# Performance work log

Hardware: AMD Instinct MI355X
Metric: run time of the kernel (lower is better)

The kernel has to match this reference:

```python
import jax, jax.numpy as jnp
import numpy as np

EPS = 1e-5
V = 65536      # number of surface vertices
E = 1048576    # number of neighbor points (~16 per vertex)
H = 128        # h_dim
CHEM_IN = 34   # 2 + num_gdf*2
GEOM_IN = 48   # num_gdf*2 + num_signatures


def _bn(x, p):
    # p: [4, dim] = (gamma, beta, running_mean, running_var); eval-mode BatchNorm1d
    g, b, m, v = p[0], p[1], p[2], p[3]
    return (x - m) * jax.lax.rsqrt(v + EPS) * g + b


def _mk_bn(key, dim):
    km, kv = jax.random.split(key)
    gamma = jnp.ones((dim,), jnp.float32)
    beta = jnp.zeros((dim,), jnp.float32)
    mean = 0.1 * jax.random.normal(km, (dim,), jnp.float32)
    var = 0.5 + jax.random.uniform(kv, (dim,), jnp.float32)  # strictly positive
    return jnp.stack([gamma, beta, mean, var])


def _mk_lin(key, din, dout):
    kw, kb = jax.random.split(key)
    s = 1.0 / np.sqrt(din)
    w = jax.random.uniform(kw, (din, dout), jnp.float32, -s, s)
    b = jax.random.uniform(kb, (dout,), jnp.float32, -s, s)
    return w, b


def setup_inputs() -> dict:
    key = jax.random.key(0)
    ks = jax.random.split(key, 16)
    chem_feats = jax.random.normal(ks[0], (E, CHEM_IN), jnp.float32)
    geom_feats = jax.random.normal(ks[1], (V, GEOM_IN), jnp.float32)
    nbr_vids = jax.random.randint(ks[2], (E,), 0, V, jnp.int64 if jax.config.jax_enable_x64 else jnp.int32)
    w1, b1 = _mk_lin(ks[3], CHEM_IN, H)
    w2, b2 = _mk_lin(ks[4], H, 2 * H)
    wg1, bg1 = _mk_lin(ks[5], GEOM_IN, H // 2)
    wg2, bg2 = _mk_lin(ks[6], H // 2, H // 2)
    wf1, bf1 = _mk_lin(ks[7], H + H // 2, H)
    wf2, bf2 = _mk_lin(ks[8], H, H)
    return {
        "chem_feats": chem_feats, "geom_feats": geom_feats, "nbr_vids": nbr_vids,
        "w1": w1, "b1": b1, "bn1": _mk_bn(ks[9], H),
        "w2": w2, "b2": b2, "bn2": _mk_bn(ks[10], 2 * H),
        "wg1": wg1, "bg1": bg1, "bng1": _mk_bn(ks[11], H // 2),
        "wg2": wg2, "bg2": bg2, "bng2": _mk_bn(ks[12], H // 2),
        "wf1": wf1, "bf1": bf1, "bnf1": _mk_bn(ks[13], H),
        "wf2": wf2, "bf2": bf2, "bnf2": _mk_bn(ks[14], H),
    }


def reference(chem_feats, geom_feats, nbr_vids,
              w1, b1, bn1, w2, b2, bn2,
              wg1, bg1, bng1, wg2, bg2, bng2,
              wf1, bf1, bnf1, wf2, bf2, bnf2):
    n_verts = geom_feats.shape[0]
    # chem_mlp: Linear -> (Dropout eval=id) -> BN -> SiLU -> Linear -> BN
    h = jax.nn.silu(_bn(chem_feats @ w1 + b1, bn1))
    h = _bn(h @ w2 + b2, bn2)                      # [E, 2H]
    nbr_filter, nbr_core = jnp.split(h, 2, axis=-1)
    h_chem = jax.nn.sigmoid(nbr_filter) * jax.nn.softplus(nbr_core)  # gated [E, H]
    h_chem = jax.ops.segment_sum(h_chem, nbr_vids, num_segments=n_verts)  # [V, H]
    # geom_mlp
    g = jax.nn.silu(_bn(geom_feats @ wg1 + bg1, bng1))
    h_geom = _bn(g @ wg2 + bg2, bng2)              # [V, H/2]
    # feat_mlp on concat
    x = jnp.concatenate([h_chem, h_geom], axis=-1)  # [V, 3H/2]
    x = jax.nn.silu(_bn(x @ wf1 + bf1, bnf1))
    h_out = _bn(x @ wf2 + bf2, bnf2)               # [V, H]
    return h_out
```

## Files before the change

### kernel.cpp

```cpp
#include <hip/hip_runtime.h>
#include <cstddef>

constexpr int V_CNT = 65536;
constexpr int E_CNT = 1048576;
constexpr int H_DIM = 128;
constexpr int CI = 34;
constexpr int GI = 48;
#define EPSF 1e-5f

typedef _Float16 f16;
typedef f16 f16x8 __attribute__((ext_vector_type(8)));
typedef float f32x4 __attribute__((ext_vector_type(4)));
#define MFMA16(a,b,c) __builtin_amdgcn_mfma_f32_16x16x32_f16(a,b,c,0,0,0)

__device__ __forceinline__ float sigmoidf_(float x){ return 1.0f/(1.0f+__expf(-x)); }
__device__ __forceinline__ float siluf_(float x){ return x/(1.0f+__expf(-x)); }
__device__ __forceinline__ float softplusf_(float x){
  return fmaxf(x,0.0f) + __logf(1.0f + __expf(-fabsf(x)));
}

__global__ __launch_bounds__(256) void prep_kernel(
    const float* __restrict__ w1, const float* __restrict__ b1, const float* __restrict__ bn1,
    const float* __restrict__ w2, const float* __restrict__ b2, const float* __restrict__ bn2,
    const float* __restrict__ wg1, const float* __restrict__ bg1, const float* __restrict__ bng1,
    const float* __restrict__ wg2, const float* __restrict__ bg2, const float* __restrict__ bng2,
    const float* __restrict__ wf1, const float* __restrict__ bf1, const float* __restrict__ bnf1,
    const float* __restrict__ wf2, const float* __restrict__ bf2, const float* __restrict__ bnf2,
    f16* __restrict__ w1f, float* __restrict__ shift1,
    f16* __restrict__ w2f, float* __restrict__ shift2,
    f16* __restrict__ wg1f, float* __restrict__ shiftg1,
    f16* __restrict__ wg2f, float* __restrict__ shiftg2,
    f16* __restrict__ wf1f, float* __restrict__ shiftf1,
    f16* __restrict__ wf2f, float* __restrict__ shiftf2)
{
  int t = blockIdx.x*256 + threadIdx.x;
  if (t < 128*64){
    int n = t>>6, k = t&63;
    float s = bn1[n]*rsqrtf(bn1[384+n]+EPSF);
    w1f[t] = (k<CI) ? (f16)(w1[k*128+n]*s) : (f16)0.f;
    if (k==0) shift1[n] = fmaf(s, b1[n]-bn1[256+n], bn1[128+n]);
  }
  if (t < 256*128){
    int n = t>>7, k = t&127;
    float s = bn2[n]*rsqrtf(bn2[768+n]+EPSF);
    w2f[t] = (f16)(w2[k*256+n]*s);
    if (k==0) shift2[n] = fmaf(s, b2[n]-bn2[512+n], bn2[256+n]);
  }
  if (t < 64*64){
    int n = t>>6, k = t&63;
    float s = bng1[n]*rsqrtf(bng1[192+n]+EPSF);
    wg1f[t] = (k<GI) ? (f16)(wg1[k*64+n]*s) : (f16)0.f;
    if (k==0) shiftg1[n] = fmaf(s, bg1[n]-bng1[128+n], bng1[64+n]);
  }
  if (t < 64*64){
    int n = t>>6, k = t&63;
    float s = bng2[n]*rsqrtf(bng2[192+n]+EPSF);
    wg2f[t] = (f16)(wg2[k*64+n]*s);
    if (k==0) shiftg2[n] = fmaf(s, bg2[n]-bng2[128+n], bng2[64+n]);
  }
  if (t < 128*192){
    int n = t/192, k = t - n*192;
    float s = bnf1[n]*rsqrtf(bnf1[384+n]+EPSF);
    wf1f[t] = (f16)(wf1[k*128+n]*s);
    if (k==0) shiftf1[n] = fmaf(s, bf1[n]-bnf1[256+n], bnf1[128+n]);
  }
  if (t < 128*128){
    int n = t>>7, k = t&127;
    float s = bnf2[n]*rsqrtf(bnf2[384+n]+EPSF);
    wf2f[t] = (f16)(wf2[k*128+n]*s);
    if (k==0) shiftf2[n] = fmaf(s, bf2[n]-bnf2[256+n], bnf2[128+n]);
  }
}

__global__ __launch_bounds__(256) void hist_kernel(const int* __restrict__ vids, int* __restrict__ counts){
  int i = blockIdx.x*blockDim.x + threadIdx.x;
  int stride = gridDim.x*blockDim.x;
  for(; i<E_CNT; i+=stride) atomicAdd(&counts[vids[i]], 1);
}

__global__ __launch_bounds__(1024) void scan_kernel(const int* __restrict__ counts,
                                                    int* __restrict__ offsets,
                                                    int* __restrict__ offsets_work){
  __shared__ int ps[1024];
  const int t = threadIdx.x;
  int4 c[16]; int s = 0;
  const int4* cp = (const int4*)counts + (size_t)t*16;
  #pragma unroll
  for(int i=0;i<16;i++){ c[i]=cp[i]; s += c[i].x+c[i].y+c[i].z+c[i].w; }
  ps[t]=s; __syncthreads();
  for(int d=1; d<1024; d<<=1){
    int v = (t>=d) ? ps[t-d] : 0;
    __syncthreads();
    ps[t] += v;
    __syncthreads();
  }
  int run = ps[t]-s;
  int4* o1 = (int4*)offsets + (size_t)t*16;
  int4* o2 = (int4*)offsets_work + (size_t)t*16;
  #pragma unroll
  for(int i=0;i<16;i++){
    int4 cc=c[i]; int4 o;
    o.x=run; run+=cc.x; o.y=run; run+=cc.y; o.z=run; run+=cc.z; o.w=run; run+=cc.w;
    o1[i]=o; o2[i]=o;
  }
  if(t==1023) offsets[65536] = run;
}

__global__ __launch_bounds__(256) void scatter_kernel(const int* __restrict__ vids,
                                                      int* __restrict__ offsets_work,
                                                      int* __restrict__ perm,
                                                      int* __restrict__ svid){
  int i = blockIdx.x*blockDim.x + threadIdx.x;
  int stride = gridDim.x*blockDim.x;
  for(; i<E_CNT; i+=stride){
    int v = vids[i];
    int pos = atomicAdd(&offsets_work[v], 1);
    perm[pos] = i;
    svid[pos] = v;
  }
}

__global__ __launch_bounds__(256) void geom_mfma(
    const float* __restrict__ geom,
    const f16* __restrict__ wg1f, const float* __restrict__ shg1,
    const f16* __restrict__ wg2f, const float* __restrict__ shg2,
    f16* __restrict__ dst, int stride, int colbase)
{
  __shared__ __align__(16) f16 Ag[64][72];
  const int t = threadIdx.x, w = t>>6, lane = t&63, n16 = lane&15, quad = lane>>4;
  const int v0 = blockIdx.x*64;
  const int col = w*16 + n16;

  for(int i=t;i<64*GI;i+=256){ int r=i/GI, k=i-r*GI; Ag[r][k] = (f16)geom[(size_t)v0*GI + i]; }
  { uint* Aw=(uint*)Ag; for(int i=t;i<64*8;i+=256){ int r=i>>3; Aw[r*36+24+(i&7)]=0u; } }

  f16x8 bg1[2], bg2[2];
  #pragma unroll
  for(int ks=0;ks<2;ks++){
    bg1[ks] = *(const f16x8*)(wg1f + (size_t)col*64 + ks*32 + quad*8);
    bg2[ks] = *(const f16x8*)(wg2f + (size_t)col*64 + ks*32 + quad*8);
  }
  __syncthreads();

  f32x4 c1[4];
  #pragma unroll
  for(int mt=0;mt<4;mt++) c1[mt] = (f32x4)(0.f);
  #pragma unroll
  for(int mt=0;mt<4;mt++)
    #pragma unroll
    for(int ks=0;ks<2;ks++){
      f16x8 a = *(const f16x8*)(&Ag[mt*16+n16][ks*32+quad*8]);
      c1[mt] = MFMA16(a, bg1[ks], c1[mt]);
    }
  __syncthreads();

  float s1 = shg1[col];
  #pragma unroll
  for(int mt=0;mt<4;mt++)
    #pragma unroll
    for(int r=0;r<4;r++)
      Ag[mt*16+quad*4+r][col] = (f16)siluf_(c1[mt][r] + s1);
  __syncthreads();

  f32x4 c2[4];
  #pragma unroll
  for(int mt=0;mt<4;mt++) c2[mt] = (f32x4)(0.f);
  #pragma unroll
  for(int mt=0;mt<4;mt++)
    #pragma unroll
    for(int ks=0;ks<2;ks++){
      f16x8 a = *(const f16x8*)(&Ag[mt*16+n16][ks*32+quad*8]);
      c2[mt] = MFMA16(a, bg2[ks], c2[mt]);
    }
  float s2 = shg2[col];
  #pragma unroll
  for(int mt=0;mt<4;mt++)
    #pragma unroll
    for(int r=0;r<4;r++)
      dst[(size_t)(v0 + mt*16+quad*4+r)*stride + colbase + col] = (f16)(c2[mt][r] + s2);
}

__global__ __launch_bounds__(256) void zero_f4(float4* p, int n4){
  int i = blockIdx.x*blockDim.x + threadIdx.x;
  int stride = gridDim.x*blockDim.x;
  float4 z; z.x=0.f; z.y=0.f; z.z=0.f; z.w=0.f;
  for(; i<n4; i+=stride) p[i] = z;
}

__global__ __launch_bounds__(256) void chem_fused(
    const float* __restrict__ chem,
    const int* __restrict__ perm, const int* __restrict__ svid,
    const f16* __restrict__ w1f, const float* __restrict__ shift1,
    const f16* __restrict__ w2f, const float* __restrict__ shift2,
    float* __restrict__ h_chem)
{
  __shared__ __align__(16) f16 A2[64][136];
  __shared__ __align__(16) f16 G[64][136];
  __shared__ int vid_s[64];
  const int t = threadIdx.x, w = t>>6, lane = t&63, n16 = lane&15, quad = lane>>4;
  const long p0 = (long)blockIdx.x*64;

  if(t<64) vid_s[t] = svid[p0+t];

  f16x8 b1[2][2];
  #pragma unroll
  for(int p=0;p<2;p++){
    int col = (2*w+p)*16 + n16;
    #pragma unroll
    for(int ks=0;ks<2;ks++)
      b1[p][ks] = *(const f16x8*)(w1f + (size_t)col*64 + ks*32 + quad*8);
  }
  float sh1v[2] = { shift1[(2*w+0)*16+n16], shift1[(2*w+1)*16+n16] };

  int pe[4];
  #pragma unroll
  for(int mt=0;mt<4;mt++) pe[mt] = perm[p0 + mt*16 + n16];

  f32x4 c1[4][2];
  #pragma unroll
  for(int mt=0;mt<4;mt++){ c1[mt][0]=(f32x4)(0.f); c1[mt][1]=(f32x4)(0.f); }
  #pragma unroll
  for(int mt=0;mt<4;mt++){
    const float* base = chem + (size_t)pe[mt]*CI;
    float2 u0 = *(const float2*)(base + quad*8 + 0);
    float2 u1 = *(const float2*)(base + quad*8 + 2);
    float2 u2 = *(const float2*)(base + quad*8 + 4);
    float2 u3 = *(const float2*)(base + quad*8 + 6);
    f16x8 a0;
    a0[0]=(f16)u0.x; a0[1]=(f16)u0.y; a0[2]=(f16)u1.x; a0[3]=(f16)u1.y;
    a0[4]=(f16)u2.x; a0[5]=(f16)u2.y; a0[6]=(f16)u3.x; a0[7]=(f16)u3.y;
    f16x8 a1 = (f16x8)(f16)0.f;
    if(quad==0){
      float2 uT = *(const float2*)(base + 32);
      a1[0]=(f16)uT.x; a1[1]=(f16)uT.y;
    }
    #pragma unroll
    for(int p=0;p<2;p++){
      c1[mt][p] = MFMA16(a0, b1[p][0], c1[mt][p]);
      c1[mt][p] = MFMA16(a1, b1[p][1], c1[mt][p]);
    }
  }
  #pragma unroll
  for(int mt=0;mt<4;mt++)
    #pragma unroll
    for(int p=0;p<2;p++){
      int col = (2*w+p)*16 + n16;
      #pragma unroll
      for(int r=0;r<4;r++)
        A2[mt*16+quad*4+r][col] = (f16)siluf_(c1[mt][p][r] + sh1v[p]);
    }
  __syncthreads();

  #pragma unroll 1
  for(int p=0;p<2;p++){
    const int gf = 2*w + p, gc = gf + 8;
    f16x8 b2f[4], b2c[4];
    #pragma unroll
    for(int ks=0;ks<4;ks++){
      b2f[ks] = *(const f16x8*)(w2f + (size_t)(gf*16+n16)*128 + ks*32 + quad*8);
      b2c[ks] = *(const f16x8*)(w2f + (size_t)(gc*16+n16)*128 + ks*32 + quad*8);
    }
    float shf = shift2[gf*16+n16];
    float shc = shift2[128 + gf*16+n16];
    f32x4 cf[4], cc_[4];
    #pragma unroll
    for(int mt=0;mt<4;mt++){ cf[mt]=(f32x4)(0.f); cc_[mt]=(f32x4)(0.f); }
    #pragma unroll
    for(int ks=0;ks<4;ks++){
      f16x8 a[4];
      #pragma unroll
      for(int mt=0;mt<4;mt++)
        a[mt] = *(const f16x8*)(&A2[mt*16+n16][ks*32+quad*8]);
      #pragma unroll
      for(int mt=0;mt<4;mt++){
        cf[mt]  = MFMA16(a[mt], b2f[ks], cf[mt]);
        cc_[mt] = MFMA16(a[mt], b2c[ks], cc_[mt]);
      }
    }
    #pragma unroll
    for(int mt=0;mt<4;mt++)
      #pragma unroll
      for(int r=0;r<4;r++){
        float f  = sigmoidf_(cf[mt][r]  + shf);
        float s  = softplusf_(cc_[mt][r] + shc);
        G[mt*16+quad*4+r][gf*16+n16] = (f16)(f*s);
      }
  }
  __syncthreads();

  {
    const int l = lane, g = w;
    const int e_beg = g*16, e_end = e_beg+16;
    float a0=0.f, a1=0.f;
    int cur = vid_s[e_beg];
    #pragma unroll 1
    for(int e=e_beg; e<e_end; ++e){
      int v = vid_s[e];
      if(v != cur){
        unsafeAtomicAdd(h_chem + (size_t)cur*H_DIM + 2*l,     a0);
        unsafeAtomicAdd(h_chem + (size_t)cur*H_DIM + 2*l + 1, a1);
        a0=0.f; a1=0.f; cur=v;
      }
      union{uint u; f16 h[2];} q;
      q.u = *(const uint*)&G[e][2*l];
      a0 += (float)q.h[0]; a1 += (float)q.h[1];
    }
    unsafeAtomicAdd(h_chem + (size_t)cur*H_DIM + 2*l,     a0);
    unsafeAtomicAdd(h_chem + (size_t)cur*H_DIM + 2*l + 1, a1);
  }
}

__global__ __launch_bounds__(256) void chem_atomic(
    const float* __restrict__ chem, const int* __restrict__ vids,
    const f16* __restrict__ w1f, const float* __restrict__ shift1,
    const f16* __restrict__ w2f, const float* __restrict__ shift2,
    float* __restrict__ h_chem)
{
  __shared__ __align__(16) f16 A2[64][136];
  __shared__ __align__(16) int vid_s[64];
  const int t = threadIdx.x, w = t>>6, lane = t&63, n16 = lane&15, quad = lane>>4;
  const long e0 = (long)blockIdx.x*64;

  if(t<64) vid_s[t] = vids[e0+t];

  f16x8 b1[2][2];
  #pragma unroll
  for(int p=0;p<2;p++){
    int col = (2*w+p)*16 + n16;
    #pragma unroll
    for(int ks=0;ks<2;ks++)
      b1[p][ks] = *(const f16x8*)(w1f + (size_t)col*64 + ks*32 + quad*8);
  }
  float sh1v[2] = { shift1[(2*w+0)*16+n16], shift1[(2*w+1)*16+n16] };

  f32x4 c1[4][2];
  #pragma unroll
  for(int mt=0;mt<4;mt++){ c1[mt][0]=(f32x4)(0.f); c1[mt][1]=(f32x4)(0.f); }
  #pragma unroll
  for(int mt=0;mt<4;mt++){
    const float* base = chem + (size_t)(e0 + mt*16 + n16)*CI;
    float2 u0 = *(const float2*)(base + quad*8 + 0);
    float2 u1 = *(const float2*)(base + quad*8 + 2);
    float2 u2 = *(const float2*)(base + quad*8 + 4);
    float2 u3 = *(const float2*)(base + quad*8 + 6);
    f16x8 a0;
    a0[0]=(f16)u0.x; a0[1]=(f16)u0.y; a0[2]=(f16)u1.x; a0[3]=(f16)u1.y;
    a0[4]=(f16)u2.x; a0[5]=(f16)u2.y; a0[6]=(f16)u3.x; a0[7]=(f16)u3.y;
    f16x8 a1 = (f16x8)(f16)0.f;
    if(quad==0){
      float2 uT = *(const float2*)(base + 32);
      a1[0]=(f16)uT.x; a1[1]=(f16)uT.y;
    }
    #pragma unroll
    for(int p=0;p<2;p++){
      c1[mt][p] = MFMA16(a0, b1[p][0], c1[mt][p]);
      c1[mt][p] = MFMA16(a1, b1[p][1], c1[mt][p]);
    }
  }
  #pragma unroll
  for(int mt=0;mt<4;mt++)
    #pragma unroll
    for(int p=0;p<2;p++){
      int col = (2*w+p)*16 + n16;
      #pragma unroll
      for(int r=0;r<4;r++)
        A2[mt*16+quad*4+r][col] = (f16)siluf_(c1[mt][p][r] + sh1v[p]);
    }
  const int ntab[4] = {2*w, 2*w+1, 2*w+8, 2*w+9};
  f16x8 b2[4][4];
  #pragma unroll
  for(int p=0;p<4;p++){
    int col = ntab[p]*16 + n16;
    #pragma unroll
    for(int ks=0;ks<4;ks++)
      b2[p][ks] = *(const f16x8*)(w2f + (size_t)col*128 + ks*32 + quad*8);
  }
  float shf[2] = { shift2[(2*w+0)*16+n16], shift2[(2*w+1)*16+n16] };
  float shc[2] = { shift2[128+(2*w+0)*16+n16], shift2[128+(2*w+1)*16+n16] };
  __syncthreads();

  f32x4 c2[4][4];
  #pragma unroll
  for(int mt=0;mt<4;mt++)
    #pragma unroll
    for(int p=0;p<4;p++) c2[mt][p] = (f32x4)(0.f);
  #pragma unroll
  for(int ks=0;ks<4;ks++){
    f16x8 a[4];
    #pragma unroll
    for(int mt=0;mt<4;mt++)
      a[mt] = *(const f16x8*)(&A2[mt*16+n16][ks*32+quad*8]);
    #pragma unroll
    for(int mt=0;mt<4;mt++)
      #pragma unroll
      for(int p=0;p<4;p++)
        c2[mt][p] = MFMA16(a[mt], b2[p][ks], c2[mt][p]);
  }
  #pragma unroll
  for(int mt=0;mt<4;mt++){
    int4 ev = *(const int4*)&vid_s[mt*16 + quad*4];
    int evv[4] = {ev.x, ev.y, ev.z, ev.w};
    #pragma unroll
    for(int p=0;p<2;p++){
      int colf = (2*w+p)*16 + n16;
      #pragma unroll
      for(int r=0;r<4;r++){
        float f  = sigmoidf_(c2[mt][p][r]   + shf[p]);
        float cc = softplusf_(c2[mt][p+2][r] + shc[p]);
        unsafeAtomicAdd(h_chem + (size_t)evv[r]*H_DIM + colf, f*cc);
      }
    }
  }
}

__global__ __launch_bounds__(256) void feat_split(
    const float* __restrict__ h_chem, const f16* __restrict__ h_geom,
    const f16* __restrict__ wf1f, const float* __restrict__ shf1,
    const f16* __restrict__ wf2f, const float* __restrict__ shf2,
    float* __restrict__ out)
{
  __shared__ __align__(16) f16 Af[64][200];
  const int t = threadIdx.x, w = t>>6, lane = t&63, n16 = lane&15, quad = lane>>4;
  const int v0 = blockIdx.x*64;

  for(int i=t;i<64*128;i+=256){ int r=i>>7, k=i&127; Af[r][k] = (f16)h_chem[(size_t)(v0+r)*128 + k]; }
  for(int i=t;i<64*64;i+=256){ int r=i>>6, k=i&63; Af[r][128+k] = h_geom[(size_t)(v0+r)*64 + k]; }

  f16x8 B1[2][6];
  #pragma unroll
  for(int p=0;p<2;p++){
    int col = (2*w+p)*16 + n16;
    #pragma unroll
    for(int ks=0;ks<6;ks++)
      B1[p][ks] = *(const f16x8*)(wf1f + (size_t)col*192 + ks*32 + quad*8);
  }
  __syncthreads();

  f32x4 c1[4][2];
  #pragma unroll
  for(int mt=0;mt<4;mt++){ c1[mt][0]=(f32x4)(0.f); c1[mt][1]=(f32x4)(0.f); }
  #pragma unroll
  for(int ks=0;ks<6;ks++){
    f16x8 a[4];
    #pragma unroll
    for(int mt=0;mt<4;mt++)
      a[mt] = *(const f16x8*)(&Af[mt*16+n16][ks*32+quad*8]);
    #pragma unroll
    for(int mt=0;mt<4;mt++)
      #pragma unroll
      for(int p=0;p<2;p++) c1[mt][p] = MFMA16(a[mt], B1[p][ks], c1[mt][p]);
  }
  __syncthreads();

  float s1v[2] = { shf1[(2*w+0)*16+n16], shf1[(2*w+1)*16+n16] };
  #pragma unroll
  for(int mt=0;mt<4;mt++)
    #pragma unroll
    for(int p=0;p<2;p++){
      int col = (2*w+p)*16 + n16;
      #pragma unroll
      for(int r=0;r<4;r++)
        Af[mt*16+quad*4+r][col] = (f16)siluf_(c1[mt][p][r] + s1v[p]);
    }
  __syncthreads();

  f16x8 B2[2][4];
  #pragma unroll
  for(int p=0;p<2;p++){
    int col = (2*w+p)*16 + n16;
    #pragma unroll
    for(int ks=0;ks<4;ks++)
      B2[p][ks] = *(const f16x8*)(wf2f + (size_t)col*128 + ks*32 + quad*8);
  }
  f32x4 c2[4][2];
  #pragma unroll
  for(int mt=0;mt<4;mt++){ c2[mt][0]=(f32x4)(0.f); c2[mt][1]=(f32x4)(0.f); }
  #pragma unroll
  for(int ks=0;ks<4;ks++){
    f16x8 a[4];
    #pragma unroll
    for(int mt=0;mt<4;mt++)
      a[mt] = *(const f16x8*)(&Af[mt*16+n16][ks*32+quad*8]);
    #pragma unroll
    for(int mt=0;mt<4;mt++)
      #pragma unroll
      for(int p=0;p<2;p++) c2[mt][p] = MFMA16(a[mt], B2[p][ks], c2[mt][p]);
  }
  float s2v[2] = { shf2[(2*w+0)*16+n16], shf2[(2*w+1)*16+n16] };
  #pragma unroll
  for(int mt=0;mt<4;mt++)
    #pragma unroll
    for(int p=0;p<2;p++){
      int col = (2*w+p)*16 + n16;
      #pragma unroll
      for(int r=0;r<4;r++)
        out[(size_t)(v0 + mt*16+quad*4+r)*128 + col] = c2[mt][p][r] + s2v[p];
    }
}

extern "C" void kernel_launch(void* const* d_in, const int* in_sizes, int n_in,
                              void* d_out, int out_size, void* d_ws, size_t ws_size,
                              hipStream_t stream) {
  const float* chem = (const float*)d_in[0];
  const float* geom = (const float*)d_in[1];
  const int*   vids = (const int*)d_in[2];
  const float* w1  = (const float*)d_in[3];
  const float* b1  = (const float*)d_in[4];
  const float* bn1 = (const float*)d_in[5];
  const float* w2  = (const float*)d_in[6];
  const float* b2  = (const float*)d_in[7];
  const float* bn2 = (const float*)d_in[8];
  const float* wg1 = (const float*)d_in[9];
  const float* bg1 = (const float*)d_in[10];
  const float* bng1= (const float*)d_in[11];
  const float* wg2 = (const float*)d_in[12];
  const float* bg2 = (const float*)d_in[13];
  const float* bng2= (const float*)d_in[14];
  const float* wf1 = (const float*)d_in[15];
  const float* bf1 = (const float*)d_in[16];
  const float* bnf1= (const float*)d_in[17];
  const float* wf2 = (const float*)d_in[18];
  const float* bf2 = (const float*)d_in[19];
  const float* bnf2= (const float*)d_in[20];
  float* out = (float*)d_out;
  char* ws = (char*)d_ws;

  const size_t NEED_BIG = 51301632ULL;
  const bool big = (ws_size >= NEED_BIG);

  if (big) {
    float* h_chem     = (float*)(ws + 0);
    f16*   h_geom     = (f16*)  (ws + 33554432);
    int*   perm       = (int*)  (ws + 41943040);
    int*   svid       = (int*)  (ws + 46137344);
    int*   counts     = (int*)  (ws + 50331648);
    int*   offsets    = (int*)  (ws + 50593792);
    int*   offsets_wk = (int*)  (ws + 50856192);
    char*  wb         = ws + 51118336;
    f16*   w1f  = (f16*)(wb);
    f16*   w2f  = (f16*)(wb + 16384);
    f16*   wg1f = (f16*)(wb + 81920);
    f16*   wg2f = (f16*)(wb + 90112);
    f16*   wf1f = (f16*)(wb + 98304);
    f16*   wf2f = (f16*)(wb + 147456);
    float* shift1  = (float*)(wb + 180224);
    float* shift2  = (float*)(wb + 180736);
    float* shiftg1 = (float*)(wb + 181760);
    float* shiftg2 = (float*)(wb + 182016);
    float* shiftf1 = (float*)(wb + 182272);
    float* shiftf2 = (float*)(wb + 182784);

    hipMemsetAsync(counts, 0, 65536*sizeof(int), stream);
    prep_kernel<<<dim3(128), dim3(256), 0, stream>>>(
        w1,b1,bn1, w2,b2,bn2, wg1,bg1,bng1, wg2,bg2,bng2, wf1,bf1,bnf1, wf2,bf2,bnf2,
        w1f,shift1, w2f,shift2, wg1f,shiftg1, wg2f,shiftg2, wf1f,shiftf1, wf2f,shiftf2);
    hist_kernel<<<dim3(1024), dim3(256), 0, stream>>>(vids, counts);
    scan_kernel<<<dim3(1), dim3(1024), 0, stream>>>(counts, offsets, offsets_wk);
    scatter_kernel<<<dim3(1024), dim3(256), 0, stream>>>(vids, offsets_wk, perm, svid);
    zero_f4<<<dim3(4096), dim3(256), 0, stream>>>((float4*)h_chem, V_CNT*H_DIM/4);
    geom_mfma<<<dim3(V_CNT/64), dim3(256), 0, stream>>>(geom, wg1f,shiftg1, wg2f,shiftg2, h_geom, 64, 0);
    chem_fused<<<dim3(E_CNT/64), dim3(256), 0, stream>>>(chem, perm, svid, w1f,shift1, w2f,shift2, h_chem);
    feat_split<<<dim3(V_CNT/64), dim3(256), 0, stream>>>(h_chem, h_geom, wf1f,shiftf1, wf2f,shiftf2, out);
  } else {
    float* h_chem = (float*)(ws + 0);
    f16*   h_geom = (f16*)  (ws + 33554432);
    char*  wb     = ws + 41943040;
    f16*   w1f  = (f16*)(wb);
    f16*   w2f  = (f16*)(wb + 16384);
    f16*   wg1f = (f16*)(wb + 81920);
    f16*   wg2f = (f16*)(wb + 90112);
    f16*   wf1f = (f16*)(wb + 98304);
    f16*   wf2f = (f16*)(wb + 147456);
    float* shift1  = (float*)(wb + 180224);
    float* shift2  = (float*)(wb + 180736);
    float* shiftg1 = (float*)(wb + 181760);
    float* shiftg2 = (float*)(wb + 182016);
    float* shiftf1 = (float*)(wb + 182272);
    float* shiftf2 = (float*)(wb + 182784);

    prep_kernel<<<dim3(128), dim3(256), 0, stream>>>(
        w1,b1,bn1, w2,b2,bn2, wg1,bg1,bng1, wg2,bg2,bng2, wf1,bf1,bnf1, wf2,bf2,bnf2,
        w1f,shift1, w2f,shift2, wg1f,shiftg1, wg2f,shiftg2, wf1f,shiftf1, wf2f,shiftf2);
    zero_f4<<<dim3(4096), dim3(256), 0, stream>>>((float4*)h_chem, V_CNT*H_DIM/4);
    geom_mfma<<<dim3(V_CNT/64), dim3(256), 0, stream>>>(geom, wg1f,shiftg1, wg2f,shiftg2, h_geom, 64, 0);
    chem_atomic<<<dim3(E_CNT/64), dim3(256), 0, stream>>>(chem, vids, w1f,shift1, w2f,shift2, h_chem);
    feat_split<<<dim3(V_CNT/64), dim3(256), 0, stream>>>(h_chem, h_geom, wf1f,shiftf1, wf2f,shiftf2, out);
  }
}
```

Measured before the change: 724.9 us.

## Fuse prep/hist/zero launches, merge geom into chem kernel, shrink feat tile

Folds weight prep, the histogram, and zeroing of h_chem into one front kernel selected by block range. The geom MLP is merged into the chem kernel as extra blocks, and the svid and offsets arrays are dropped in favour of vids[perm]. Gate results are kept in registers so the chem kernel reuses the A2 shared buffer, cutting LDS and raising occupancy. The feat kernel drops to 32-row tiles, loads use float4, and sigmoid/silu use a fast reciprocal. Fewer launches and less memory traffic are traded for an extra indirect load and slightly lower rcp precision.

Result: faster. 692.7 us (-4.4%).

```diff
diff --git a/kernel.cpp b/kernel.cpp
--- a/kernel.cpp
+++ b/kernel.cpp
@@ -13,13 +13,14 @@
 typedef float f32x4 __attribute__((ext_vector_type(4)));
 #define MFMA16(a,b,c) __builtin_amdgcn_mfma_f32_16x16x32_f16(a,b,c,0,0,0)
 
-__device__ __forceinline__ float sigmoidf_(float x){ return 1.0f/(1.0f+__expf(-x)); }
-__device__ __forceinline__ float siluf_(float x){ return x/(1.0f+__expf(-x)); }
+__device__ __forceinline__ float frcp_(float x){ return __builtin_amdgcn_rcpf(x); }
+__device__ __forceinline__ float sigmoidf_(float x){ return frcp_(1.0f+__expf(-x)); }
+__device__ __forceinline__ float siluf_(float x){ return x*frcp_(1.0f+__expf(-x)); }
 __device__ __forceinline__ float softplusf_(float x){
   return fmaxf(x,0.0f) + __logf(1.0f + __expf(-fabsf(x)));
 }
 
-__global__ __launch_bounds__(256) void prep_kernel(
+__global__ __launch_bounds__(256) void front_kernel(
     const float* __restrict__ w1, const float* __restrict__ b1, const float* __restrict__ bn1,
     const float* __restrict__ w2, const float* __restrict__ b2, const float* __restrict__ bn2,
     const float* __restrict__ wg1, const float* __restrict__ bg1, const float* __restrict__ bng1,
@@ -31,9 +32,24 @@
     f16* __restrict__ wg1f, float* __restrict__ shiftg1,
     f16* __restrict__ wg2f, float* __restrict__ shiftg2,
     f16* __restrict__ wf1f, float* __restrict__ shiftf1,
-    f16* __restrict__ wf2f, float* __restrict__ shiftf2)
+    f16* __restrict__ wf2f, float* __restrict__ shiftf2,
+    const int* __restrict__ vids, int* __restrict__ counts,
+    float4* __restrict__ h_chem_zero)
 {
-  int t = blockIdx.x*256 + threadIdx.x;
+  const int b = blockIdx.x;
+  if (b >= 1152) {
+    int i = (b-1152)*256 + threadIdx.x;
+    float4 z; z.x=0.f; z.y=0.f; z.z=0.f; z.w=0.f;
+    const int n4 = V_CNT*H_DIM/4;
+    for(; i<n4; i+=2048*256) h_chem_zero[i] = z;
+    return;
+  }
+  if (b >= 128) {
+    int i = (b-128)*256 + threadIdx.x;
+    for(; i<E_CNT; i+=1024*256) atomicAdd(&counts[vids[i]], 1);
+    return;
+  }
+  int t = b*256 + threadIdx.x;
   if (t < 128*64){
     int n = t>>6, k = t&63;
     float s = bn1[n]*rsqrtf(bn1[384+n]+EPSF);
@@ -72,14 +88,7 @@
   }
 }
 
-__global__ __launch_bounds__(256) void hist_kernel(const int* __restrict__ vids, int* __restrict__ counts){
-  int i = blockIdx.x*blockDim.x + threadIdx.x;
-  int stride = gridDim.x*blockDim.x;
-  for(; i<E_CNT; i+=stride) atomicAdd(&counts[vids[i]], 1);
-}
-
 __global__ __launch_bounds__(1024) void scan_kernel(const int* __restrict__ counts,
-                                                    int* __restrict__ offsets,
                                                     int* __restrict__ offsets_work){
   __shared__ int ps[1024];
   const int t = threadIdx.x;
@@ -95,28 +104,24 @@
     __syncthreads();
   }
   int run = ps[t]-s;
-  int4* o1 = (int4*)offsets + (size_t)t*16;
   int4* o2 = (int4*)offsets_work + (size_t)t*16;
   #pragma unroll
   for(int i=0;i<16;i++){
     int4 cc=c[i]; int4 o;
     o.x=run; run+=cc.x; o.y=run; run+=cc.y; o.z=run; run+=cc.z; o.w=run; run+=cc.w;
-    o1[i]=o; o2[i]=o;
-  }
-  if(t==1023) offsets[65536] = run;
+    o2[i]=o;
+  }
 }
 
 __global__ __launch_bounds__(256) void scatter_kernel(const int* __restrict__ vids,
                                                       int* __restrict__ offsets_work,
-                                                      int* __restrict__ perm,
-                                                      int* __restrict__ svid){
+                                                      int* __restrict__ perm){
   int i = blockIdx.x*blockDim.x + threadIdx.x;
   int stride = gridDim.x*blockDim.x;
   for(; i<E_CNT; i+=stride){
     int v = vids[i];
     int pos = atomicAdd(&offsets_work[v], 1);
     perm[pos] = i;
-    svid[pos] = v;
   }
 }
 
@@ -124,7 +129,7 @@
     const float* __restrict__ geom,
     const f16* __restrict__ wg1f, const float* __restrict__ shg1,
     const f16* __restrict__ wg2f, const float* __restrict__ shg2,
-    f16* __restrict__ dst, int stride, int colbase)
+    f16* __restrict__ dst)
 {
   __shared__ __align__(16) f16 Ag[64][72];
   const int t = threadIdx.x, w = t>>6, lane = t&63, n16 = lane&15, quad = lane>>4;
@@ -177,30 +182,80 @@
   for(int mt=0;mt<4;mt++)
     #pragma unroll
     for(int r=0;r<4;r++)
-      dst[(size_t)(v0 + mt*16+quad*4+r)*stride + colbase + col] = (f16)(c2[mt][r] + s2);
-}
-
-__global__ __launch_bounds__(256) void zero_f4(float4* p, int n4){
-  int i = blockIdx.x*blockDim.x + threadIdx.x;
-  int stride = gridDim.x*blockDim.x;
-  float4 z; z.x=0.f; z.y=0.f; z.z=0.f; z.w=0.f;
-  for(; i<n4; i+=stride) p[i] = z;
-}
-
-__global__ __launch_bounds__(256) void chem_fused(
-    const float* __restrict__ chem,
-    const int* __restrict__ perm, const int* __restrict__ svid,
+      dst[(size_t)(v0 + mt*16+quad*4+r)*64 + col] = (f16)(c2[mt][r] + s2);
+}
+
+__global__ __launch_bounds__(256) void chem_geom(
+    const float* __restrict__ chem, const float* __restrict__ geom,
+    const int* __restrict__ perm, const int* __restrict__ vids,
     const f16* __restrict__ w1f, const float* __restrict__ shift1,
     const f16* __restrict__ w2f, const float* __restrict__ shift2,
-    float* __restrict__ h_chem)
+    const f16* __restrict__ wg1f, const float* __restrict__ shg1,
+    const f16* __restrict__ wg2f, const float* __restrict__ shg2,
+    float* __restrict__ h_chem, f16* __restrict__ h_geom)
 {
   __shared__ __align__(16) f16 A2[64][136];
-  __shared__ __align__(16) f16 G[64][136];
   __shared__ int vid_s[64];
   const int t = threadIdx.x, w = t>>6, lane = t&63, n16 = lane&15, quad = lane>>4;
-  const long p0 = (long)blockIdx.x*64;
-
-  if(t<64) vid_s[t] = svid[p0+t];
+
+  if (blockIdx.x < 1024) {
+    f16 (*Ag)[72] = reinterpret_cast<f16(*)[72]>(&A2[0][0]);
+    const int v0 = blockIdx.x*64;
+    const int col = w*16 + n16;
+
+    for(int i=t;i<64*GI;i+=256){ int r=i/GI, k=i-r*GI; Ag[r][k] = (f16)geom[(size_t)v0*GI + i]; }
+    { uint* Aw=(uint*)&Ag[0][0]; for(int i=t;i<64*8;i+=256){ int r=i>>3; Aw[r*36+24+(i&7)]=0u; } }
+
+    f16x8 bg1[2], bg2[2];
+    #pragma unroll
+    for(int ks=0;ks<2;ks++){
+      bg1[ks] = *(const f16x8*)(wg1f + (size_t)col*64 + ks*32 + quad*8);
+      bg2[ks] = *(const f16x8*)(wg2f + (size_t)col*64 + ks*32 + quad*8);
+    }
+    __syncthreads();
+
+    f32x4 c1[4];
+    #pragma unroll
+    for(int mt=0;mt<4;mt++) c1[mt] = (f32x4)(0.f);
+    #pragma unroll
+    for(int mt=0;mt<4;mt++)
+      #pragma unroll
+      for(int ks=0;ks<2;ks++){
+        f16x8 a = *(const f16x8*)(&Ag[mt*16+n16][ks*32+quad*8]);
+        c1[mt] = MFMA16(a, bg1[ks], c1[mt]);
+      }
+    __syncthreads();
+
+    float s1 = shg1[col];
+    #pragma unroll
+    for(int mt=0;mt<4;mt++)
+      #pragma unroll
+      for(int r=0;r<4;r++)
+        Ag[mt*16+quad*4+r][col] = (f16)siluf_(c1[mt][r] + s1);
+    __syncthreads();
+
+    f32x4 c2[4];
+    #pragma unroll
+    for(int mt=0;mt<4;mt++) c2[mt] = (f32x4)(0.f);
+    #pragma unroll
+    for(int mt=0;mt<4;mt++)
+      #pragma unroll
+      for(int ks=0;ks<2;ks++){
+        f16x8 a = *(const f16x8*)(&Ag[mt*16+n16][ks*32+quad*8]);
+        c2[mt] = MFMA16(a, bg2[ks], c2[mt]);
+      }
+    float s2 = shg2[col];
+    #pragma unroll
+    for(int mt=0;mt<4;mt++)
+      #pragma unroll
+      for(int r=0;r<4;r++)
+        h_geom[(size_t)(v0 + mt*16+quad*4+r)*64 + col] = (f16)(c2[mt][r] + s2);
+    return;
+  }
+
+  const long p0 = (long)(blockIdx.x - 1024)*64;
+
+  if(t<64) vid_s[t] = vids[perm[p0+t]];
 
   f16x8 b1[2][2];
   #pragma unroll
@@ -222,13 +277,11 @@
   #pragma unroll
   for(int mt=0;mt<4;mt++){
     const float* base = chem + (size_t)pe[mt]*CI;
-    float2 u0 = *(const float2*)(base + quad*8 + 0);
-    float2 u1 = *(const float2*)(base + quad*8 + 2);
-    float2 u2 = *(const float2*)(base + quad*8 + 4);
-    float2 u3 = *(const float2*)(base + quad*8 + 6);
+    float4 u0 = *(const float4*)(base + quad*8 + 0);
+    float4 u1 = *(const float4*)(base + quad*8 + 4);
     f16x8 a0;
-    a0[0]=(f16)u0.x; a0[1]=(f16)u0.y; a0[2]=(f16)u1.x; a0[3]=(f16)u1.y;
-    a0[4]=(f16)u2.x; a0[5]=(f16)u2.y; a0[6]=(f16)u3.x; a0[7]=(f16)u3.y;
+    a0[0]=(f16)u0.x; a0[1]=(f16)u0.y; a0[2]=(f16)u0.z; a0[3]=(f16)u0.w;
+    a0[4]=(f16)u1.x; a0[5]=(f16)u1.y; a0[6]=(f16)u1.z; a0[7]=(f16)u1.w;
     f16x8 a1 = (f16x8)(f16)0.f;
     if(quad==0){
       float2 uT = *(const float2*)(base + 32);
@@ -251,8 +304,8 @@
     }
   __syncthreads();
 
-  #pragma unroll 1
-  for(int p=0;p<2;p++){
+  uint gp0[8], gp1[8];
+  auto l2pass = [&](const int p, uint* __restrict__ gp){
     const int gf = 2*w + p, gc = gf + 8;
     f16x8 b2f[4], b2c[4];
     #pragma unroll
@@ -280,12 +333,32 @@
     #pragma unroll
     for(int mt=0;mt<4;mt++)
       #pragma unroll
-      for(int r=0;r<4;r++){
-        float f  = sigmoidf_(cf[mt][r]  + shf);
-        float s  = softplusf_(cc_[mt][r] + shc);
-        G[mt*16+quad*4+r][gf*16+n16] = (f16)(f*s);
+      for(int j=0;j<2;j++){
+        float f0 = sigmoidf_(cf[mt][2*j]  +shf);
+        float s0 = softplusf_(cc_[mt][2*j]  +shc);
+        float f1 = sigmoidf_(cf[mt][2*j+1]+shf);
+        float s1 = softplusf_(cc_[mt][2*j+1]+shc);
+        union{uint u; f16 h[2];} q;
+        q.h[0]=(f16)(f0*s0); q.h[1]=(f16)(f1*s1);
+        gp[mt*2+j] = q.u;
       }
-  }
+  };
+  l2pass(0, gp0);
+  l2pass(1, gp1);
+  __syncthreads();
+
+  #pragma unroll
+  for(int mt=0;mt<4;mt++)
+    #pragma unroll
+    for(int j=0;j<2;j++){
+      union{uint u; f16 h[2];} q0, q1;
+      q0.u = gp0[mt*2+j]; q1.u = gp1[mt*2+j];
+      int row = mt*16+quad*4+2*j;
+      A2[row  ][(2*w+0)*16+n16] = q0.h[0];
+      A2[row+1][(2*w+0)*16+n16] = q0.h[1];
+      A2[row  ][(2*w+1)*16+n16] = q1.h[0];
+      A2[row+1][(2*w+1)*16+n16] = q1.h[1];
+    }
   __syncthreads();
 
   {
@@ -302,7 +375,7 @@
         a0=0.f; a1=0.f; cur=v;
       }
       union{uint u; f16 h[2];} q;
-      q.u = *(const uint*)&G[e][2*l];
+      q.u = *(const uint*)&A2[e][2*l];
       a0 += (float)q.h[0]; a1 += (float)q.h[1];
     }
     unsafeAtomicAdd(h_chem + (size_t)cur*H_DIM + 2*l,     a0);
@@ -339,13 +412,11 @@
   #pragma unroll
   for(int mt=0;mt<4;mt++){
     const float* base = chem + (size_t)(e0 + mt*16 + n16)*CI;
-    float2 u0 = *(const float2*)(base + quad*8 + 0);
-    float2 u1 = *(const float2*)(base + quad*8 + 2);
-    float2 u2 = *(const float2*)(base + quad*8 + 4);
-    float2 u3 = *(const float2*)(base + quad*8 + 6);
+    float4 u0 = *(const float4*)(base + quad*8 + 0);
+    float4 u1 = *(const float4*)(base + quad*8 + 4);
     f16x8 a0;
-    a0[0]=(f16)u0.x; a0[1]=(f16)u0.y; a0[2]=(f16)u1.x; a0[3]=(f16)u1.y;
-    a0[4]=(f16)u2.x; a0[5]=(f16)u2.y; a0[6]=(f16)u3.x; a0[7]=(f16)u3.y;
+    a0[0]=(f16)u0.x; a0[1]=(f16)u0.y; a0[2]=(f16)u0.z; a0[3]=(f16)u0.w;
+    a0[4]=(f16)u1.x; a0[5]=(f16)u1.y; a0[6]=(f16)u1.z; a0[7]=(f16)u1.w;
     f16x8 a1 = (f16x8)(f16)0.f;
     if(quad==0){
       float2 uT = *(const float2*)(base + 32);
@@ -413,18 +484,18 @@
   }
 }
 
-__global__ __launch_bounds__(256) void feat_split(
+__global__ __launch_bounds__(256) void feat32(
     const float* __restrict__ h_chem, const f16* __restrict__ h_geom,
     const f16* __restrict__ wf1f, const float* __restrict__ shf1,
     const f16* __restrict__ wf2f, const float* __restrict__ shf2,
     float* __restrict__ out)
 {
-  __shared__ __align__(16) f16 Af[64][200];
+  __shared__ __align__(16) f16 Af[32][200];
   const int t = threadIdx.x, w = t>>6, lane = t&63, n16 = lane&15, quad = lane>>4;
-  const int v0 = blockIdx.x*64;
-
-  for(int i=t;i<64*128;i+=256){ int r=i>>7, k=i&127; Af[r][k] = (f16)h_chem[(size_t)(v0+r)*128 + k]; }
-  for(int i=t;i<64*64;i+=256){ int r=i>>6, k=i&63; Af[r][128+k] = h_geom[(size_t)(v0+r)*64 + k]; }
+  const int v0 = blockIdx.x*32;
+
+  for(int i=t;i<32*128;i+=256){ int r=i>>7, k=i&127; Af[r][k] = (f16)h_chem[(size_t)(v0+r)*128 + k]; }
+  for(int i=t;i<32*64;i+=256){ int r=i>>6, k=i&63; Af[r][128+k] = h_geom[(size_t)(v0+r)*64 + k]; }
 
   f16x8 B1[2][6];
   #pragma unroll
@@ -436,17 +507,17 @@
   }
   __syncthreads();
 
-  f32x4 c1[4][2];
-  #pragma unroll
-  for(int mt=0;mt<4;mt++){ c1[mt][0]=(f32x4)(0.f); c1[mt][1]=(f32x4)(0.f); }
+  f32x4 c1[2][2];
+  #pragma unroll
+  for(int mt=0;mt<2;mt++){ c1[mt][0]=(f32x4)(0.f); c1[mt][1]=(f32x4)(0.f); }
   #pragma unroll
   for(int ks=0;ks<6;ks++){
-    f16x8 a[4];
-    #pragma unroll
-    for(int mt=0;mt<4;mt++)
+    f16x8 a[2];
+    #pragma unroll
+    for(int mt=0;mt<2;mt++)
       a[mt] = *(const f16x8*)(&Af[mt*16+n16][ks*32+quad*8]);
     #pragma unroll
-    for(int mt=0;mt<4;mt++)
+    for(int mt=0;mt<2;mt++)
       #pragma unroll
       for(int p=0;p<2;p++) c1[mt][p] = MFMA16(a[mt], B1[p][ks], c1[mt][p]);
   }
@@ -454,7 +525,7 @@
 
   float s1v[2] = { shf1[(2*w+0)*16+n16], shf1[(2*w+1)*16+n16] };
   #pragma unroll
-  for(int mt=0;mt<4;mt++)
+  for(int mt=0;mt<2;mt++)
     #pragma unroll
     for(int p=0;p<2;p++){
       int col = (2*w+p)*16 + n16;
@@ -472,23 +543,23 @@
     for(int ks=0;ks<4;ks++)
       B2[p][ks] = *(const f16x8*)(wf2f + (size_t)col*128 + ks*32 + quad*8);
   }
-  f32x4 c2[4][2];
-  #pragma unroll
-  for(int mt=0;mt<4;mt++){ c2[mt][0]=(f32x4)(0.f); c2[mt][1]=(f32x4)(0.f); }
+  f32x4 c2[2][2];
+  #pragma unroll
+  for(int mt=0;mt<2;mt++){ c2[mt][0]=(f32x4)(0.f); c2[mt][1]=(f32x4)(0.f); }
   #pragma unroll
   for(int ks=0;ks<4;ks++){
-    f16x8 a[4];
-    #pragma unroll
-    for(int mt=0;mt<4;mt++)
+    f16x8 a[2];
+    #pragma unroll
+    for(int mt=0;mt<2;mt++)
       a[mt] = *(const f16x8*)(&Af[mt*16+n16][ks*32+quad*8]);
     #pragma unroll
-    for(int mt=0;mt<4;mt++)
+    for(int mt=0;mt<2;mt++)
       #pragma unroll
       for(int p=0;p<2;p++) c2[mt][p] = MFMA16(a[mt], B2[p][ks], c2[mt][p]);
   }
   float s2v[2] = { shf2[(2*w+0)*16+n16], shf2[(2*w+1)*16+n16] };
   #pragma unroll
-  for(int mt=0;mt<4;mt++)
+  for(int mt=0;mt<2;mt++)
     #pragma unroll
     for(int p=0;p<2;p++){
       int col = (2*w+p)*16 + n16;
@@ -525,18 +596,16 @@
   float* out = (float*)d_out;
   char* ws = (char*)d_ws;
 
-  const size_t NEED_BIG = 51301632ULL;
+  const size_t NEED_BIG = 46850048ULL;
   const bool big = (ws_size >= NEED_BIG);
 
   if (big) {
     float* h_chem     = (float*)(ws + 0);
     f16*   h_geom     = (f16*)  (ws + 33554432);
     int*   perm       = (int*)  (ws + 41943040);
-    int*   svid       = (int*)  (ws + 46137344);
-    int*   counts     = (int*)  (ws + 50331648);
-    int*   offsets    = (int*)  (ws + 50593792);
-    int*   offsets_wk = (int*)  (ws + 50856192);
-    char*  wb         = ws + 51118336;
+    int*   counts     = (int*)  (ws + 46137344);
+    int*   offsets_wk = (int*)  (ws + 46399488);
+    char*  wb         = ws + 46661632;
     f16*   w1f  = (f16*)(wb);
     f16*   w2f  = (f16*)(wb + 16384);
     f16*   wg1f = (f16*)(wb + 81920);
@@ -551,16 +620,15 @@
     float* shiftf2 = (float*)(wb + 182784);
 
     hipMemsetAsync(counts, 0, 65536*sizeof(int), stream);
-    prep_kernel<<<dim3(128), dim3(256), 0, stream>>>(
+    front_kernel<<<dim3(3200), dim3(256), 0, stream>>>(
         w1,b1,bn1, w2,b2,bn2, wg1,bg1,bng1, wg2,bg2,bng2, wf1,bf1,bnf1, wf2,bf2,bnf2,
-        w1f,shift1, w2f,shift2, wg1f,shiftg1, wg2f,shiftg2, wf1f,shiftf1, wf2f,shiftf2);
-    hist_kernel<<<dim3(1024), dim3(256), 0, stream>>>(vids, counts);
-    scan_kernel<<<dim3(1), dim3(1024), 0, stream>>>(counts, offsets, offsets_wk);
-    scatter_kernel<<<dim3(1024), dim3(256), 0, stream>>>(vids, offsets_wk, perm, svid);
-    zero_f4<<<dim3(4096), dim3(256), 0, stream>>>((float4*)h_chem, V_CNT*H_DIM/4);
-    geom_mfma<<<dim3(V_CNT/64), dim3(256), 0, stream>>>(geom, wg1f,shiftg1, wg2f,shiftg2, h_geom, 64, 0);
-    chem_fused<<<dim3(E_CNT/64), dim3(256), 0, stream>>>(chem, perm, svid, w1f,shift1, w2f,shift2, h_chem);
-    feat_split<<<dim3(V_CNT/64), dim3(256), 0, stream>>>(h_chem, h_geom, wf1f,shiftf1, wf2f,shiftf2, out);
+        w1f,shift1, w2f,shift2, wg1f,shiftg1, wg2f,shiftg2, wf1f,shiftf1, wf2f,shiftf2,
+        vids, counts, (float4*)h_chem);
+    scan_kernel<<<dim3(1), dim3(1024), 0, stream>>>(counts, offsets_wk);
+    scatter_kernel<<<dim3(1024), dim3(256), 0, stream>>>(vids, offsets_wk, perm);
+    chem_geom<<<dim3(1024 + E_CNT/64), dim3(256), 0, stream>>>(chem, geom, perm, vids,
+        w1f,shift1, w2f,shift2, wg1f,shiftg1, wg2f,shiftg2, h_chem, h_geom);
+    feat32<<<dim3(V_CNT/32), dim3(256), 0, stream>>>(h_chem, h_geom, wf1f,shiftf1, wf2f,shiftf2, out);
   } else {
     float* h_chem = (float*)(ws + 0);
     f16*   h_geom = (f16*)  (ws + 33554432);
@@ -578,12 +646,13 @@
     float* shiftf1 = (float*)(wb + 182272);
     float* shiftf2 = (float*)(wb + 182784);
 
-    prep_kernel<<<dim3(128), dim3(256), 0, stream>>>(
+    hipMemsetAsync(h_chem, 0, (size_t)V_CNT*H_DIM*sizeof(float), stream);
+    front_kernel<<<dim3(128), dim3(256), 0, stream>>>(
         w1,b1,bn1, w2,b2,bn2, wg1,bg1,bng1, wg2,bg2,bng2, wf1,bf1,bnf1, wf2,bf2,bnf2,
-        w1f,shift1, w2f,shift2, wg1f,shiftg1, wg2f,shiftg2, wf1f,shiftf1, wf2f,shiftf2);
-    zero_f4<<<dim3(4096), dim3(256), 0, stream>>>((float4*)h_chem, V_CNT*H_DIM/4);
-    geom_mfma<<<dim3(V_CNT/64), dim3(256), 0, stream>>>(geom, wg1f,shiftg1, wg2f,shiftg2, h_geom, 64, 0);
+        w1f,shift1, w2f,shift2, wg1f,shiftg1, wg2f,shiftg2, wf1f,shiftf1, wf2f,shiftf2,
+        vids, nullptr, nullptr);
+    geom_mfma<<<dim3(V_CNT/64), dim3(256), 0, stream>>>(geom, wg1f,shiftg1, wg2f,shiftg2, h_geom);
     chem_atomic<<<dim3(E_CNT/64), dim3(256), 0, stream>>>(chem, vids, w1f,shift1, w2f,shift2, h_chem);
-    feat_split<<<dim3(V_CNT/64), dim3(256), 0, stream>>>(h_chem, h_geom, wf1f,shiftf1, wf2f,shiftf2, out);
-  }
-}
+    feat32<<<dim3(V_CNT/32), dim3(256), 0, stream>>>(h_chem, h_geom, wf1f,shiftf1, wf2f,shiftf2, out);
+  }
+}
```
